# Performance work log

Hardware: AMD Instinct MI355X
Metric: run time of the kernel (lower is better)

The kernel has to match this reference:

```python
import jax, jax.numpy as jnp
import numpy as np

A = 64        # atom_fea_len
NBR = 41      # nbr_fea_len
ORIG = 92     # orig_atom_fea_len
NCONV = 3
N = 50000     # total atoms
M = 12        # neighbors per atom
B = 1000      # crystals
NPC = 50      # atoms per crystal (B*NPC == N)
EPS = 1e-5


def setup_inputs() -> dict:
    key = jax.random.key(0)
    ks = jax.random.split(key, 16)
    s = lambda k, shape: (jax.random.normal(k, shape, jnp.float32) * 0.05)
    inp = {
        "atom_fea": jax.random.normal(ks[0], (N, ORIG), jnp.float32),
        "nbr_fea": jax.random.uniform(ks[1], (N, M, NBR), dtype=jnp.float32),
        "nbr_fea_idx": jax.random.randint(ks[2], (N, M), 0, N),
        "crystal_atom_idx": jnp.arange(B * NPC).reshape(B, NPC),
        # params (weights stored as (in, out) so fwd is x @ w + b)
        "emb_w": s(ks[3], (ORIG, A)),
        "fc_full_w": s(ks[4], (NCONV, 2 * A + NBR, 2 * A)),
        "fc_full_b": s(ks[5], (NCONV, 2 * A)),
        "bn1_g": jnp.ones((NCONV, 2 * A), jnp.float32),
        "bn1_b": jnp.zeros((NCONV, 2 * A), jnp.float32),
        "bn2_g": jnp.ones((NCONV, A), jnp.float32),
        "bn2_b": jnp.zeros((NCONV, A), jnp.float32),
        "adj_w": s(ks[6], (6, A, A)),   # torch Bilinear weight (out, in1, in2)
        "adj_b": s(ks[7], (6,)),
        "fc1_w": s(ks[8], (6, 6)),
        "fc1_b": s(ks[9], (6,)),
        "af_w": s(ks[10], (A, ORIG)),
        "af_b": s(ks[11], (ORIG,)),
    }
    return inp


def _batchnorm(x, g, b):
    # training-mode BN over axis 0 (torch default biased variance)
    m = jnp.mean(x, axis=0)
    v = jnp.var(x, axis=0)
    return (x - m) * jax.lax.rsqrt(v + EPS) * g + b


def _conv_layer(x, nbr_fea, nbr_idx, w, b, g1, b1, g2, b2):
    n, m = nbr_idx.shape
    atom_nbr = x[nbr_idx]  # (N, M, A) gather
    total = jnp.concatenate(
        [jnp.broadcast_to(x[:, None, :], (n, m, A)), atom_nbr, nbr_fea], axis=2
    )  # (N, M, 2A+NBR)
    gated = total @ w + b  # (N, M, 2A)
    gated = _batchnorm(gated.reshape(-1, 2 * A), g1, b1).reshape(n, m, 2 * A)
    nbr_filter, nbr_core = gated[..., :A], gated[..., A:]
    summed = jnp.sum(jax.nn.sigmoid(nbr_filter) * jax.nn.softplus(nbr_core), axis=1)
    summed = _batchnorm(summed, g2, b2)
    return jax.nn.softplus(x + summed)


def reference(atom_fea, nbr_fea, nbr_fea_idx, crystal_atom_idx, emb_w,
              fc_full_w, fc_full_b, bn1_g, bn1_b, bn2_g, bn2_b,
              adj_w, adj_b, fc1_w, fc1_b, af_w, af_b):
    x = atom_fea @ emb_w  # embedding, no bias
    for i in range(NCONV):
        x = _conv_layer(x, nbr_fea, nbr_fea_idx,
                        fc_full_w[i], fc_full_b[i],
                        bn1_g[i], bn1_b[i], bn2_g[i], bn2_b[i])
    cf = x[crystal_atom_idx]  # (B, NPC, A)
    # Original code bug: fc_adj(x1, x2) is called with x1 == x2 == tiled atom
    # features, so pair (i, j) depends only on atom j. Compute per-atom bilinear
    # then tile -> identical output.
    q = jnp.einsum('bnd,ode,bne->bno', cf, adj_w, cf) + adj_b  # (B, NPC, 6)
    q = q @ fc1_w + fc1_b
    logp = jax.nn.log_softmax(q, axis=-1)  # row-wise over the 6 classes
    edge_prob = jnp.broadcast_to(logp[:, None, :, :], (B, NPC, NPC, 6)).reshape(B, NPC * NPC, 6)
    atom_feature = cf @ af_w + af_b  # (B, NPC, ORIG)
    return edge_prob, atom_feature
```

## Files before the change

kernel.cpp:

```cpp
#include <hip/hip_runtime.h>
#include <hip/hip_bf16.h>

#define AA 64
#define NBRF 41
#define ORIGD 92
#define NATOM 50000
#define MM 12
#define NB 1000
#define NPCC 50
#define NEDGE (NATOM*MM)
#define NREP 64
constexpr float EPS_BN = 1e-5f;

using bf16 = __hip_bfloat16;
typedef short s16x8 __attribute__((ext_vector_type(8)));
typedef float f32x4 __attribute__((ext_vector_type(4)));

__device__ __forceinline__ float u2f(unsigned short u) {
    union { float f; unsigned int i; } v; v.i = ((unsigned int)u) << 16; return v.f;
}
__device__ __forceinline__ unsigned short f2bu(float f) {
    bf16 h = __float2bfloat16(f);
    return *reinterpret_cast<unsigned short*>(&h);
}
__device__ __forceinline__ float fsigmoid(float x) {
    float e = __expf(-x);
    return __builtin_amdgcn_rcpf(1.f + e);
}
__device__ __forceinline__ float fsoftplus(float x) {
    return fmaxf(x, 0.f) + __logf(1.f + __expf(-fabsf(x)));
}

#define GLD16(g, l)                                                              \
    __builtin_amdgcn_global_load_lds(                                            \
        (const __attribute__((address_space(1))) unsigned int*)(g),              \
        (__attribute__((address_space(3))) unsigned int*)(l), 16, 0, 0)

__global__ void k_prep0(const float* __restrict__ W, unsigned short* __restrict__ Wt,
                        float* __restrict__ stats, int nstat) {
    int b = blockIdx.x, t = threadIdx.x;
    if (b < 3) {
        for (int i = t; i < 9216; i += 256) {
            int n = i / 72, k = i - n * 72;
            float v = 0.f;
            if (b == 0)      { if (k < NBRF) v = W[(128 + k) * 128 + n]; }
            else if (b == 1) { if (k < 64)   v = W[(64 + k) * 128 + n]; }
            else             { if (k < 64)   v = W[k * 128 + n]; }
            Wt[b * 9216 + i] = f2bu(v);
        }
    } else {
        int base = (b - 3) * 2048;
        for (int i = t; i < 2048; i += 256) {
            int idx = base + i;
            if (idx < nstat) stats[idx] = 0.f;
        }
    }
}

__global__ void k_prepQ(const float* __restrict__ adjw, unsigned short* __restrict__ Bq) {
    int i = blockIdx.x * 256 + threadIdx.x;
    if (i >= 384 * 72) return;
    int n = i / 72, k = i - n * 72;
    float v = (k < 64) ? adjw[(n >> 6) * 4096 + k * 64 + (n & 63)] : 0.f;
    Bq[i] = f2bu(v);
}

__global__ __launch_bounds__(256) void k_embed(const float* __restrict__ af,
                                               const float* __restrict__ w,
                                               float* __restrict__ x,
                                               unsigned short* __restrict__ xb) {
    __shared__ float wl[ORIGD * AA];
    __shared__ float al[4][ORIGD];
    int t = threadIdx.x;
    for (int i = t; i < ORIGD * AA; i += 256) wl[i] = w[i];
    int n0 = blockIdx.x * 4;
    for (int i = t; i < 4 * ORIGD; i += 256) {
        int a = i / ORIGD, k = i - a * ORIGD;
        al[a][k] = af[(size_t)(n0 + a) * ORIGD + k];
    }
    __syncthreads();
    int c = t & 63, a = t >> 6;
    float acc = 0.f;
    #pragma unroll 4
    for (int k = 0; k < ORIGD; ++k)
        acc += al[a][k] * wl[k * AA + c];
    size_t idx = (size_t)(n0 + a) * AA + c;
    x[idx] = acc;
    xb[idx] = f2bu(acc);
}


#define MFMA_PH1(acc)                                                               \
    _Pragma("unroll")                                                               \
    for (int mt = 0; mt < 3; ++mt) {                                                \
        int mrow = w * 48 + mt * 16 + ln;                                           \
        s16x8 a0 = *reinterpret_cast<const s16x8*>(&Al[mrow * 72 + quad * 8]);      \
        s16x8 a1 = *reinterpret_cast<const s16x8*>(&Al[mrow * 72 + quad * 8 + 32]); \
        _Pragma("unroll")                                                           \
        for (int nt = 0; nt < 8; ++nt) {                                            \
            int nrow = nt * 16 + ln;                                                \
            s16x8 b0 = *reinterpret_cast<const s16x8*>(&Bl[nrow * 72 + quad * 8]);  \
            s16x8 b1 = *reinterpret_cast<const s16x8*>(&Bl[nrow * 72 + quad * 8 + 32]); \
            acc[mt][nt] = __builtin_amdgcn_mfma_f32_16x16x32_bf16(a0, b0, acc[mt][nt], 0, 0, 0); \
            acc[mt][nt] = __builtin_amdgcn_mfma_f32_16x16x32_bf16(a1, b1, acc[mt][nt], 0, 0, 0); \
        }                                                                           \
    }

__global__ __launch_bounds__(256, 2) void k_passA(const unsigned short* __restrict__ xb,
                                                  const float* __restrict__ nf,
                                                  const unsigned short* __restrict__ Wt,
                                                  const int* __restrict__ nidx,
                                                  float* __restrict__ stats,
                                                  uint4* __restrict__ gated) {
    __shared__ __attribute__((aligned(16))) unsigned char SMEM[72704];
    unsigned short* Al = reinterpret_cast<unsigned short*>(SMEM);
    unsigned short* Ax = Al + 192 * 72;
    unsigned short* As = Ax + 192 * 64;
    unsigned short* Bl = As + 16 * 64;
    int t = threadIdx.x;
    int n0 = blockIdx.x * 16;
    int w = t >> 6, lane = t & 63, ln = lane & 15, quad = lane >> 4;

    {
        const float* fg = nf + (size_t)n0 * MM * NBRF;
        #pragma unroll 4
        for (int i = t; i < 192 * NBRF; i += 256) {
            int m = i / NBRF, k = i - m * NBRF;
            Al[m * 72 + k] = f2bu(fg[i]);
        }
        #pragma unroll
        for (int i = t; i < 192 * 23; i += 256) {
            int m = i / 23, k = 41 + (i - m * 23);
            Al[m * 72 + k] = 0;
        }
    }
    for (int c = w; c < 18; c += 4)
        GLD16(Wt + c * 512 + lane * 8, (char*)Bl + c * 1024);
    const int* nb = nidx + n0 * MM;
    int idxv[6];
    #pragma unroll
    for (int c = 0; c < 6; ++c) idxv[c] = nb[w * 48 + c * 8 + (lane >> 3)];
    int sl = ((lane & 7) ^ ((lane >> 3) & 7)) * 8;
    __syncthreads();

    #pragma unroll
    for (int c = 0; c < 6; ++c)
        GLD16(xb + (size_t)idxv[c] * 64 + sl, (char*)Ax + (w * 48 + c * 8) * 128);
    if (w == 3) {
        GLD16(xb + (size_t)(n0 + (lane >> 3)) * 64 + sl, (char*)As);
        GLD16(xb + (size_t)(n0 + 8 + (lane >> 3)) * 64 + sl, (char*)As + 1024);
    }

    f32x4 acc[3][8];
    f32x4 z4 = {0.f, 0.f, 0.f, 0.f};
    for (int i = 0; i < 3; ++i) for (int j = 0; j < 8; ++j) acc[i][j] = z4;

    MFMA_PH1(acc);
    __syncthreads();
    for (int c = w; c < 18; c += 4)
        GLD16(Wt + 9216 + c * 512 + lane * 8, (char*)Bl + c * 1024);
    __syncthreads();

    {
        int sw0 = (quad ^ (ln & 7)) * 8, sw1 = ((quad + 4) ^ (ln & 7)) * 8;
        #pragma unroll
        for (int mt = 0; mt < 3; ++mt) {
            int mrow = w * 48 + mt * 16 + ln;
            s16x8 a0 = *reinterpret_cast<const s16x8*>(&Ax[mrow * 64 + sw0]);
            s16x8 a1 = *reinterpret_cast<const s16x8*>(&Ax[mrow * 64 + sw1]);
            #pragma unroll
            for (int nt = 0; nt < 8; ++nt) {
                int nrow = nt * 16 + ln;
                s16x8 b0 = *reinterpret_cast<const s16x8*>(&Bl[nrow * 72 + quad * 8]);
                s16x8 b1 = *reinterpret_cast<const s16x8*>(&Bl[nrow * 72 + quad * 8 + 32]);
                acc[mt][nt] = __builtin_amdgcn_mfma_f32_16x16x32_bf16(a0, b0, acc[mt][nt], 0, 0, 0);
                acc[mt][nt] = __builtin_amdgcn_mfma_f32_16x16x32_bf16(a1, b1, acc[mt][nt], 0, 0, 0);
            }
        }
    }
    __syncthreads();
    for (int c = w; c < 18; c += 4)
        GLD16(Wt + 2 * 9216 + c * 512 + lane * 8, (char*)Bl + c * 1024);
    __syncthreads();

    #pragma unroll
    for (int mt = 0; mt < 3; ++mt) {
        int mrow = w * 48 + mt * 16 + ln;
        int atom = mrow / 12;
        int s0 = (quad ^ (atom & 7)) * 8, s1 = ((quad + 4) ^ (atom & 7)) * 8;
        s16x8 a0 = *reinterpret_cast<const s16x8*>(&As[atom * 64 + s0]);
        s16x8 a1 = *reinterpret_cast<const s16x8*>(&As[atom * 64 + s1]);
        #pragma unroll
        for (int nt = 0; nt < 8; ++nt) {
            int nrow = nt * 16 + ln;
            s16x8 b0 = *reinterpret_cast<const s16x8*>(&Bl[nrow * 72 + quad * 8]);
            s16x8 b1 = *reinterpret_cast<const s16x8*>(&Bl[nrow * 72 + quad * 8 + 32]);
            acc[mt][nt] = __builtin_amdgcn_mfma_f32_16x16x32_bf16(a0, b0, acc[mt][nt], 0, 0, 0);
            acc[mt][nt] = __builtin_amdgcn_mfma_f32_16x16x32_bf16(a1, b1, acc[mt][nt], 0, 0, 0);
        }
    }

    uint4* gblk = gated + (size_t)blockIdx.x * 3072;
    float s[8] = {0,0,0,0,0,0,0,0}, q[8] = {0,0,0,0,0,0,0,0};
    #pragma unroll
    for (int mt = 0; mt < 3; ++mt) {
        #pragma unroll
        for (int reg = 0; reg < 4; ++reg) {
            float r[8];
            #pragma unroll
            for (int nt = 0; nt < 8; ++nt) {
                r[nt] = acc[mt][nt][reg];
                s[nt] += r[nt]; q[nt] += r[nt] * r[nt];
            }
            uint4 u;
            u.x = (unsigned)f2bu(r[0]) | ((unsigned)f2bu(r[1]) << 16);
            u.y = (unsigned)f2bu(r[2]) | ((unsigned)f2bu(r[3]) << 16);
            u.z = (unsigned)f2bu(r[4]) | ((unsigned)f2bu(r[5]) << 16);
            u.w = (unsigned)f2bu(r[6]) | ((unsigned)f2bu(r[7]) << 16);
            gblk[(mt * 4 + reg) * 256 + t] = u;
        }
    }
    #pragma unroll
    for (int nt = 0; nt < 8; ++nt) {
        s[nt] += __shfl_xor(s[nt], 16); s[nt] += __shfl_xor(s[nt], 32);
        q[nt] += __shfl_xor(q[nt], 16); q[nt] += __shfl_xor(q[nt], 32);
    }
    __syncthreads();
    float* red = reinterpret_cast<float*>(SMEM);
    if (quad == 0) {
        #pragma unroll
        for (int nt = 0; nt < 8; ++nt) {
            red[((w * 8 + nt) * 16 + ln) * 2 + 0] = s[nt];
            red[((w * 8 + nt) * 16 + ln) * 2 + 1] = q[nt];
        }
    }
    __syncthreads();
    {
        int c = t >> 1, j = t & 1;
        float v = 0.f;
        #pragma unroll
        for (int w2 = 0; w2 < 4; ++w2)
            v += red[((w2 * 8 + (c >> 4)) * 16 + (c & 15)) * 2 + j];
        int rep = (blockIdx.x & (NREP - 1)) << 8;
        atomicAdd(&stats[rep + j * 128 + c], v);
    }
}

__global__ void k_sc1(const float* __restrict__ stats, const float* __restrict__ g,
                      const float* __restrict__ b, float* __restrict__ sc) {
    int c = threadIdx.x;
    float s = 0.f, q = 0.f;
    for (int r = 0; r < NREP; ++r) {
        s += stats[r * 256 + c];
        q += stats[r * 256 + 128 + c];
    }
    float cnt = (float)NEDGE;
    float mean = s / cnt;
    float var = q / cnt - mean * mean;
    float inv = rsqrtf(var + EPS_BN);
    float scale = g[c] * inv;
    sc[c] = scale;
    sc[128 + c] = b[c] - mean * scale;
}

__global__ __launch_bounds__(256) void k_passBs(const uint4* __restrict__ gated,
                                                const float* __restrict__ sc,
                                                float* __restrict__ summed,
                                                float* __restrict__ stats2) {
    __shared__ unsigned short P[192 * 66];
    __shared__ float sred[512];
    int t = threadIdx.x;
    int n0 = blockIdx.x * 16;
    int w = t >> 6, lane = t & 63, ln = lane & 15, quad = lane >> 4;
    float scF[4], shF[4], scC[4], shC[4];
    #pragma unroll
    for (int nt = 0; nt < 4; ++nt) {
        int cc = nt * 16 + ln;
        scF[nt] = sc[cc];      shF[nt] = sc[128 + cc];
        scC[nt] = sc[64 + cc]; shC[nt] = sc[192 + cc];
    }
    const uint4* gblk = gated + (size_t)blockIdx.x * 3072;
    #pragma unroll
    for (int mt = 0; mt < 3; ++mt) {
        #pragma unroll
        for (int reg = 0; reg < 4; ++reg) {
            uint4 u = gblk[(mt * 4 + reg) * 256 + t];
            int m = (w * 3 + mt) * 16 + quad * 4 + reg;
            unsigned uu[4] = {u.x, u.y, u.z, u.w};
            #pragma unroll
            for (int nt = 0; nt < 4; ++nt) {
                float rfv = u2f((unsigned short)((nt & 1) ? (uu[nt >> 1] >> 16) : (uu[nt >> 1] & 0xffff)));
                float rcv = u2f((unsigned short)((nt & 1) ? (uu[2 + (nt >> 1)] >> 16) : (uu[2 + (nt >> 1)] & 0xffff)));
                float rf = rfv * scF[nt] + shF[nt];
                float rc = rcv * scC[nt] + shC[nt];
                P[m * 66 + nt * 16 + ln] = f2bu(fsigmoid(rf) * fsoftplus(rc));
            }
        }
    }
    __syncthreads();
    int cc = t & 63, who = t >> 6;
    float sA = 0.f, qA = 0.f;
    #pragma unroll
    for (int k2 = 0; k2 < 4; ++k2) {
        int a = who + k2 * 4;
        float v = 0.f;
        #pragma unroll
        for (int j = 0; j < 12; ++j) v += u2f(P[(a * 12 + j) * 66 + cc]);
        summed[(size_t)(n0 + a) * AA + cc] = v;
        sA += v; qA += v * v;
    }
    sred[who * 64 + cc] = sA;
    sred[256 + who * 64 + cc] = qA;
    __syncthreads();
    if (t < 64) {
        float s4 = sred[t] + sred[64 + t] + sred[128 + t] + sred[192 + t];
        float q4 = sred[256 + t] + sred[320 + t] + sred[384 + t] + sred[448 + t];
        int rep = (blockIdx.x & (NREP - 1)) << 7;
        atomicAdd(&stats2[rep + t], s4);
        atomicAdd(&stats2[rep + 64 + t], q4);
    }
}

__global__ void k_sc2(const float* __restrict__ stats2, const float* __restrict__ g,
                      const float* __restrict__ b, float* __restrict__ sc2) {
    int c = threadIdx.x;
    float s = 0.f, q = 0.f;
    for (int r = 0; r < NREP; ++r) {
        s += stats2[r * 128 + c];
        q += stats2[r * 128 + 64 + c];
    }
    float cnt = (float)NATOM;
    float mean = s / cnt;
    float var = q / cnt - mean * mean;
    float inv = rsqrtf(var + EPS_BN);
    float scale = g[c] * inv;
    sc2[c] = scale;
    sc2[64 + c] = b[c] - mean * scale;
}

__global__ void k_update(float* __restrict__ x, const float* __restrict__ summed,
                         const float* __restrict__ sc2, unsigned short* __restrict__ xb) {
    int i = blockIdx.x * blockDim.x + threadIdx.x;
    if (i < NATOM * AA) {
        int c = i & 63;
        float s = summed[i] * sc2[c] + sc2[64 + c];
        float v = fsoftplus(x[i] + s);
        x[i] = v;
        xb[i] = f2bu(v);
    }
}

__global__ __launch_bounds__(256) void k_q(const float* __restrict__ x, const int* __restrict__ cidx,
                                           const unsigned short* __restrict__ Bq,
                                           const float* __restrict__ adjb,
                                           const float* __restrict__ fc1w,
                                           const float* __restrict__ fc1b,
                                           float* __restrict__ logp) {
    __shared__ __attribute__((aligned(16))) unsigned short Aq[64 * 72];
    __shared__ __attribute__((aligned(16))) unsigned short Bl[384 * 72];
    __shared__ float qv[64][6];
    int t = threadIdx.x;
    int p0 = blockIdx.x * 64;
    for (int i = t; i < 64 * 72; i += 256) {
        int a = i / 72, k = i - a * 72;
        int ga = p0 + a;
        float v = (k < 64 && ga < NATOM) ? x[(size_t)cidx[ga < NATOM ? ga : 0] * AA + k] : 0.f;
        Aq[i] = f2bu(v);
    }
    for (int i = t; i < 3456; i += 256)
        reinterpret_cast<uint4*>(Bl)[i] = reinterpret_cast<const uint4*>(Bq)[i];
    __syncthreads();

    int w = t >> 6, lane = t & 63, ln = lane & 15, quad = lane >> 4;
    f32x4 acc[24];
    f32x4 z4 = {0.f, 0.f, 0.f, 0.f};
    #pragma unroll
    for (int i = 0; i < 24; ++i) acc[i] = z4;
    {
        int mrow = w * 16 + ln;
        s16x8 a0 = *reinterpret_cast<const s16x8*>(&Aq[mrow * 72 + quad * 8]);
        s16x8 a1 = *reinterpret_cast<const s16x8*>(&Aq[mrow * 72 + quad * 8 + 32]);
        #pragma unroll
        for (int nt = 0; nt < 24; ++nt) {
            int nrow = nt * 16 + ln;
            s16x8 b0 = *reinterpret_cast<const s16x8*>(&Bl[nrow * 72 + quad * 8]);
            s16x8 b1 = *reinterpret_cast<const s16x8*>(&Bl[nrow * 72 + quad * 8 + 32]);
            acc[nt] = __builtin_amdgcn_mfma_f32_16x16x32_bf16(a0, b0, acc[nt], 0, 0, 0);
            acc[nt] = __builtin_amdgcn_mfma_f32_16x16x32_bf16(a1, b1, acc[nt], 0, 0, 0);
        }
    }
    float cfv[4][4];
    #pragma unroll
    for (int reg = 0; reg < 4; ++reg) {
        int ga = p0 + w * 16 + quad * 4 + reg;
        const float* xr = x + (size_t)cidx[ga < NATOM ? ga : 0] * AA;
        #pragma unroll
        for (int et = 0; et < 4; ++et)
            cfv[reg][et] = (ga < NATOM) ? xr[et * 16 + ln] : 0.f;
    }
    float bo[6];
    #pragma unroll
    for (int o = 0; o < 6; ++o) bo[o] = adjb[o];
    #pragma unroll
    for (int reg = 0; reg < 4; ++reg) {
        #pragma unroll
        for (int o = 0; o < 6; ++o) {
            float p = 0.f;
            #pragma unroll
            for (int et = 0; et < 4; ++et)
                p += acc[o * 4 + et][reg] * cfv[reg][et];
            p += __shfl_xor(p, 1); p += __shfl_xor(p, 2);
            p += __shfl_xor(p, 4); p += __shfl_xor(p, 8);
            if (ln == 0) qv[w * 16 + quad * 4 + reg][o] = p + bo[o];
        }
    }
    __syncthreads();
    if (t < 64) {
        int ga = p0 + t;
        if (ga < NATOM) {
            float q2[6];
            float mx = -1e30f;
            #pragma unroll
            for (int o2 = 0; o2 < 6; ++o2) {
                float acc2 = fc1b[o2];
                #pragma unroll
                for (int o = 0; o < 6; ++o) acc2 += qv[t][o] * fc1w[o * 6 + o2];
                q2[o2] = acc2; mx = fmaxf(mx, acc2);
            }
            float se = 0.f;
            #pragma unroll
            for (int o2 = 0; o2 < 6; ++o2) se += __expf(q2[o2] - mx);
            float lse = mx + __logf(se);
            #pragma unroll
            for (int o2 = 0; o2 < 6; ++o2) logp[(size_t)ga * 6 + o2] = q2[o2] - lse;
        }
    }
}

__global__ void k_edge(const float* __restrict__ logp, float* __restrict__ out0) {
    int i4 = blockIdx.x * blockDim.x + threadIdx.x;
    if (i4 >= (NB * NPCC * NPCC * 6) / 4) return;
    int e = i4 * 4;
    int b = e / (NPCC * NPCC * 6);
    int rr = e - b * (NPCC * NPCC * 6);
    const float* lb = &logp[(size_t)b * NPCC * 6];
    float4 v;
    int r0 = rr % 300;       v.x = lb[r0];
    int r1 = (rr + 1) % 300; v.y = lb[r1];
    int r2 = (rr + 2) % 300; v.z = lb[r2];
    int r3 = (rr + 3) % 300; v.w = lb[r3];
    *reinterpret_cast<float4*>(&out0[e]) = v;
}

__global__ __launch_bounds__(256) void k_af(const float* __restrict__ x, const int* __restrict__ cidx,
                                            const float* __restrict__ afw,
                                            const float* __restrict__ afb,
                                            float* __restrict__ out1) {
    __shared__ float wl[AA * ORIGD];
    __shared__ float cfl[16][AA];
    __shared__ float bl[ORIGD];
    int t = threadIdx.x;
    for (int i = t; i < AA * ORIGD; i += 256) wl[i] = afw[i];
    if (t < ORIGD) bl[t] = afb[t];
    int p0 = blockIdx.x * 16;
    for (int i = t; i < 16 * AA; i += 256) {
        int a = i >> 6, e = i & 63;
        cfl[a][e] = x[(size_t)cidx[p0 + a] * AA + e];
    }
    __syncthreads();
    for (int i = t; i < 16 * ORIGD; i += 256) {
        int a = i / ORIGD, c = i - a * ORIGD;
        float acc = bl[c];
        #pragma unroll 8
        for (int k = 0; k < AA; ++k)
            acc += cfl[a][k] * wl[k * ORIGD + c];
        out1[(size_t)(p0 + a) * ORIGD + c] = acc;
    }
}

extern "C" void kernel_launch(void* const* d_in, const int* in_sizes, int n_in,
                              void* d_out, int out_size, void* d_ws, size_t ws_size,
                              hipStream_t stream) {
    (void)in_sizes; (void)n_in; (void)out_size; (void)ws_size;
    const float* atom_fea  = (const float*)d_in[0];
    const float* nbr_fea   = (const float*)d_in[1];
    const int*   nbr_idx   = (const int*)d_in[2];
    const int*   cidx      = (const int*)d_in[3];
    const float* emb_w     = (const float*)d_in[4];
    const float* fc_full_w = (const float*)d_in[5];
    const float* bn1_g = (const float*)d_in[7];
    const float* bn1_b = (const float*)d_in[8];
    const float* bn2_g = (const float*)d_in[9];
    const float* bn2_b = (const float*)d_in[10];
    const float* adj_w = (const float*)d_in[11];
    const float* adj_b = (const float*)d_in[12];
    const float* fc1_w = (const float*)d_in[13];
    const float* fc1_b = (const float*)d_in[14];
    const float* af_w  = (const float*)d_in[15];
    const float* af_b  = (const float*)d_in[16];

    float* out0 = (float*)d_out;
    float* out1 = out0 + (size_t)NB * NPCC * NPCC * 6;

    float* ws = (float*)d_ws;
    float* x      = ws;
    float* summed = x + (size_t)NATOM * AA;
    float* logp   = summed + (size_t)NATOM * AA;
    float* stats1 = logp + (size_t)NATOM * 6;
    float* stats2 = stats1 + (size_t)NREP * 256;
    float* sc1    = stats2 + (size_t)NREP * 128;
    float* sc2    = sc1 + 256;
    float* endf   = sc2 + 128;
    size_t off = (((size_t)((char*)endf - (char*)d_ws)) + 255) & ~(size_t)255;
    unsigned short* xb = (unsigned short*)((char*)d_ws + off);
    unsigned short* Wt = xb + (size_t)NATOM * 64;
    unsigned short* Bq = Wt + 3 * 9216;
    size_t goff = (off + ((size_t)NATOM * 64 + 3 * 9216 + 384 * 72) * 2 + 255) & ~(size_t)255;
    uint4* gated = (uint4*)((char*)d_ws + goff);

    const int nstat = NREP * 256 + NREP * 128;
    k_embed<<<NATOM / 4, 256, 0, stream>>>(atom_fea, emb_w, x, xb);
    k_prepQ<<<108, 256, 0, stream>>>(adj_w, Bq);
    for (int layer = 0; layer < 3; ++layer) {
        const float* W = fc_full_w + (size_t)layer * 169 * 128;
        k_prep0<<<15, 256, 0, stream>>>(W, Wt, stats1, nstat);
        k_passA<<<NATOM / 16, 256, 0, stream>>>(xb, nbr_fea, Wt, nbr_idx, stats1, gated);
        k_sc1<<<1, 128, 0, stream>>>(stats1, bn1_g + layer * 128, bn1_b + layer * 128, sc1);
        k_passBs<<<NATOM / 16, 256, 0, stream>>>(gated, sc1, summed, stats2);
        k_sc2<<<1, 64, 0, stream>>>(stats2, bn2_g + layer * 64, bn2_b + layer * 64, sc2);
        k_update<<<(NATOM * AA + 255) / 256, 256, 0, stream>>>(x, summed, sc2, xb);
    }
    k_q<<<(NATOM + 63) / 64, 256, 0, stream>>>(x, cidx, Bq, adj_b, fc1_w, fc1_b, logp);
    k_edge<<<((NB * NPCC * NPCC * 6) / 4 + 255) / 256, 256, 0, stream>>>(logp, out0);
    k_af<<<NATOM / 16, 256, 0, stream>>>(x, cidx, af_w, af_b, out1);
}
```

Measured before the change: 760.0 us.

## Pre-pack neighbor features to bf16 once and keep atom state only in bf16

Adds a one-time kernel that converts the fp32 neighbor features into a padded bf16 layout (48 per row), so each conv layer's passA loads them directly into LDS with async global-to-LDS copies instead of converting element by element three times. passA now prefetches both weight slices into separate LDS buffers up front and reuses one A buffer for the neighbor tile and then the gathered neighbor rows. The fp32 copy of x is dropped and every consumer reads the bf16 xb. This cuts HBM traffic but compounds bf16 rounding of the residual state across layers, which risks accuracy.

```diff
diff --git a/kernel.cpp b/kernel.cpp
--- a/kernel.cpp
+++ b/kernel.cpp
@@ -35,6 +35,26 @@
     __builtin_amdgcn_global_load_lds(                                            \
         (const __attribute__((address_space(1))) unsigned int*)(g),              \
         (__attribute__((address_space(3))) unsigned int*)(l), 16, 0, 0)
+
+__global__ __launch_bounds__(256) void k_prepN(const float* __restrict__ nf,
+                                               unsigned short* __restrict__ nbp) {
+    const int total = NEDGE * 6;
+    for (int i = blockIdx.x * 256 + threadIdx.x; i < total; i += gridDim.x * 256) {
+        int row = i / 6, j = i - row * 6;
+        const float* src = nf + (size_t)row * NBRF + j * 8;
+        int base = j * 8;
+        unsigned short h[8];
+        #pragma unroll
+        for (int e = 0; e < 8; ++e)
+            h[e] = (base + e < NBRF) ? f2bu(src[e]) : (unsigned short)0;
+        uint4 u;
+        u.x = (unsigned)h[0] | ((unsigned)h[1] << 16);
+        u.y = (unsigned)h[2] | ((unsigned)h[3] << 16);
+        u.z = (unsigned)h[4] | ((unsigned)h[5] << 16);
+        u.w = (unsigned)h[6] | ((unsigned)h[7] << 16);
+        *reinterpret_cast<uint4*>(nbp + (size_t)row * 48 + j * 8) = u;
+    }
+}
 
 __global__ void k_prep0(const float* __restrict__ W, unsigned short* __restrict__ Wt,
                         float* __restrict__ stats, int nstat) {
@@ -67,7 +87,6 @@
 
 __global__ __launch_bounds__(256) void k_embed(const float* __restrict__ af,
                                                const float* __restrict__ w,
-                                               float* __restrict__ x,
                                                unsigned short* __restrict__ xb) {
     __shared__ float wl[ORIGD * AA];
     __shared__ float al[4][ORIGD];
@@ -84,105 +103,85 @@
     #pragma unroll 4
     for (int k = 0; k < ORIGD; ++k)
         acc += al[a][k] * wl[k * AA + c];
-    size_t idx = (size_t)(n0 + a) * AA + c;
-    x[idx] = acc;
-    xb[idx] = f2bu(acc);
-}
-
-
-#define MFMA_PH1(acc)                                                               \
-    _Pragma("unroll")                                                               \
-    for (int mt = 0; mt < 3; ++mt) {                                                \
-        int mrow = w * 48 + mt * 16 + ln;                                           \
-        s16x8 a0 = *reinterpret_cast<const s16x8*>(&Al[mrow * 72 + quad * 8]);      \
-        s16x8 a1 = *reinterpret_cast<const s16x8*>(&Al[mrow * 72 + quad * 8 + 32]); \
-        _Pragma("unroll")                                                           \
-        for (int nt = 0; nt < 8; ++nt) {                                            \
-            int nrow = nt * 16 + ln;                                                \
-            s16x8 b0 = *reinterpret_cast<const s16x8*>(&Bl[nrow * 72 + quad * 8]);  \
-            s16x8 b1 = *reinterpret_cast<const s16x8*>(&Bl[nrow * 72 + quad * 8 + 32]); \
-            acc[mt][nt] = __builtin_amdgcn_mfma_f32_16x16x32_bf16(a0, b0, acc[mt][nt], 0, 0, 0); \
-            acc[mt][nt] = __builtin_amdgcn_mfma_f32_16x16x32_bf16(a1, b1, acc[mt][nt], 0, 0, 0); \
-        }                                                                           \
-    }
+    xb[(size_t)(n0 + a) * AA + c] = f2bu(acc);
+}
+
 
 __global__ __launch_bounds__(256, 2) void k_passA(const unsigned short* __restrict__ xb,
-                                                  const float* __restrict__ nf,
+                                                  const unsigned short* __restrict__ nbp,
                                                   const unsigned short* __restrict__ Wt,
                                                   const int* __restrict__ nidx,
                                                   float* __restrict__ stats,
                                                   uint4* __restrict__ gated) {
-    __shared__ __attribute__((aligned(16))) unsigned char SMEM[72704];
-    unsigned short* Al = reinterpret_cast<unsigned short*>(SMEM);
-    unsigned short* Ax = Al + 192 * 72;
-    unsigned short* As = Ax + 192 * 64;
-    unsigned short* Bl = As + 16 * 64;
+    __shared__ __attribute__((aligned(16))) unsigned char SMEM[63488];
+    unsigned short* A   = reinterpret_cast<unsigned short*>(SMEM);
+    unsigned short* As  = A + 192 * 64;
+    unsigned short* Bl0 = As + 16 * 64;
+    unsigned short* Bl1 = Bl0 + 128 * 72;
     int t = threadIdx.x;
     int n0 = blockIdx.x * 16;
     int w = t >> 6, lane = t & 63, ln = lane & 15, quad = lane >> 4;
 
-    {
-        const float* fg = nf + (size_t)n0 * MM * NBRF;
-        #pragma unroll 4
-        for (int i = t; i < 192 * NBRF; i += 256) {
-            int m = i / NBRF, k = i - m * NBRF;
-            Al[m * 72 + k] = f2bu(fg[i]);
-        }
-        #pragma unroll
-        for (int i = t; i < 192 * 23; i += 256) {
-            int m = i / 23, k = 41 + (i - m * 23);
-            Al[m * 72 + k] = 0;
-        }
-    }
+    const unsigned short* nbrow = nbp + (size_t)n0 * MM * 48;
     for (int c = w; c < 18; c += 4)
-        GLD16(Wt + c * 512 + lane * 8, (char*)Bl + c * 1024);
-    const int* nb = nidx + n0 * MM;
-    int idxv[6];
-    #pragma unroll
-    for (int c = 0; c < 6; ++c) idxv[c] = nb[w * 48 + c * 8 + (lane >> 3)];
+        GLD16(nbrow + c * 512 + lane * 8, (char*)A + c * 1024);
+    for (int c = w; c < 18; c += 4)
+        GLD16(Wt + c * 512 + lane * 8, (char*)Bl0 + c * 1024);
+    for (int c = w; c < 18; c += 4)
+        GLD16(Wt + 9216 + c * 512 + lane * 8, (char*)Bl1 + c * 1024);
     int sl = ((lane & 7) ^ ((lane >> 3) & 7)) * 8;
-    __syncthreads();
-
-    #pragma unroll
-    for (int c = 0; c < 6; ++c)
-        GLD16(xb + (size_t)idxv[c] * 64 + sl, (char*)Ax + (w * 48 + c * 8) * 128);
     if (w == 3) {
         GLD16(xb + (size_t)(n0 + (lane >> 3)) * 64 + sl, (char*)As);
         GLD16(xb + (size_t)(n0 + 8 + (lane >> 3)) * 64 + sl, (char*)As + 1024);
     }
+    if (t < 64) A[192 * 48 + t] = 0;
+    const int* nb = nidx + n0 * MM;
+    int idxv[6];
+    #pragma unroll
+    for (int c = 0; c < 6; ++c) idxv[c] = nb[w * 48 + c * 8 + (lane >> 3)];
+    __syncthreads();
 
     f32x4 acc[3][8];
     f32x4 z4 = {0.f, 0.f, 0.f, 0.f};
     for (int i = 0; i < 3; ++i) for (int j = 0; j < 8; ++j) acc[i][j] = z4;
-
-    MFMA_PH1(acc);
-    __syncthreads();
+    int sw0 = (quad ^ (ln & 7)) * 8, sw1 = ((quad + 4) ^ (ln & 7)) * 8;
+
+    #pragma unroll
+    for (int mt = 0; mt < 3; ++mt) {
+        int mrow = w * 48 + mt * 16 + ln;
+        s16x8 a0 = *reinterpret_cast<const s16x8*>(&A[mrow * 48 + quad * 8]);
+        s16x8 a1 = *reinterpret_cast<const s16x8*>(&A[mrow * 48 + quad * 8 + 32]);
+        #pragma unroll
+        for (int nt = 0; nt < 8; ++nt) {
+            int nrow = nt * 16 + ln;
+            s16x8 b0 = *reinterpret_cast<const s16x8*>(&Bl0[nrow * 72 + quad * 8]);
+            s16x8 b1 = *reinterpret_cast<const s16x8*>(&Bl0[nrow * 72 + quad * 8 + 32]);
+            acc[mt][nt] = __builtin_amdgcn_mfma_f32_16x16x32_bf16(a0, b0, acc[mt][nt], 0, 0, 0);
+            acc[mt][nt] = __builtin_amdgcn_mfma_f32_16x16x32_bf16(a1, b1, acc[mt][nt], 0, 0, 0);
+        }
+    }
+    __syncthreads();
+    #pragma unroll
+    for (int c = 0; c < 6; ++c)
+        GLD16(xb + (size_t)idxv[c] * 64 + sl, (char*)A + (w * 48 + c * 8) * 128);
     for (int c = w; c < 18; c += 4)
-        GLD16(Wt + 9216 + c * 512 + lane * 8, (char*)Bl + c * 1024);
-    __syncthreads();
-
-    {
-        int sw0 = (quad ^ (ln & 7)) * 8, sw1 = ((quad + 4) ^ (ln & 7)) * 8;
-        #pragma unroll
-        for (int mt = 0; mt < 3; ++mt) {
-            int mrow = w * 48 + mt * 16 + ln;
-            s16x8 a0 = *reinterpret_cast<const s16x8*>(&Ax[mrow * 64 + sw0]);
-            s16x8 a1 = *reinterpret_cast<const s16x8*>(&Ax[mrow * 64 + sw1]);
-            #pragma unroll
-            for (int nt = 0; nt < 8; ++nt) {
-                int nrow = nt * 16 + ln;
-                s16x8 b0 = *reinterpret_cast<const s16x8*>(&Bl[nrow * 72 + quad * 8]);
-                s16x8 b1 = *reinterpret_cast<const s16x8*>(&Bl[nrow * 72 + quad * 8 + 32]);
-                acc[mt][nt] = __builtin_amdgcn_mfma_f32_16x16x32_bf16(a0, b0, acc[mt][nt], 0, 0, 0);
-                acc[mt][nt] = __builtin_amdgcn_mfma_f32_16x16x32_bf16(a1, b1, acc[mt][nt], 0, 0, 0);
-            }
-        }
-    }
-    __syncthreads();
-    for (int c = w; c < 18; c += 4)
-        GLD16(Wt + 2 * 9216 + c * 512 + lane * 8, (char*)Bl + c * 1024);
-    __syncthreads();
-
+        GLD16(Wt + 2 * 9216 + c * 512 + lane * 8, (char*)Bl0 + c * 1024);
+    __syncthreads();
+
+    #pragma unroll
+    for (int mt = 0; mt < 3; ++mt) {
+        int mrow = w * 48 + mt * 16 + ln;
+        s16x8 a0 = *reinterpret_cast<const s16x8*>(&A[mrow * 64 + sw0]);
+        s16x8 a1 = *reinterpret_cast<const s16x8*>(&A[mrow * 64 + sw1]);
+        #pragma unroll
+        for (int nt = 0; nt < 8; ++nt) {
+            int nrow = nt * 16 + ln;
+            s16x8 b0 = *reinterpret_cast<const s16x8*>(&Bl1[nrow * 72 + quad * 8]);
+            s16x8 b1 = *reinterpret_cast<const s16x8*>(&Bl1[nrow * 72 + quad * 8 + 32]);
+            acc[mt][nt] = __builtin_amdgcn_mfma_f32_16x16x32_bf16(a0, b0, acc[mt][nt], 0, 0, 0);
+            acc[mt][nt] = __builtin_amdgcn_mfma_f32_16x16x32_bf16(a1, b1, acc[mt][nt], 0, 0, 0);
+        }
+    }
     #pragma unroll
     for (int mt = 0; mt < 3; ++mt) {
         int mrow = w * 48 + mt * 16 + ln;
@@ -193,8 +192,8 @@
         #pragma unroll
         for (int nt = 0; nt < 8; ++nt) {
             int nrow = nt * 16 + ln;
-            s16x8 b0 = *reinterpret_cast<const s16x8*>(&Bl[nrow * 72 + quad * 8]);
-            s16x8 b1 = *reinterpret_cast<const s16x8*>(&Bl[nrow * 72 + quad * 8 + 32]);
+            s16x8 b0 = *reinterpret_cast<const s16x8*>(&Bl0[nrow * 72 + quad * 8]);
+            s16x8 b1 = *reinterpret_cast<const s16x8*>(&Bl0[nrow * 72 + quad * 8 + 32]);
             acc[mt][nt] = __builtin_amdgcn_mfma_f32_16x16x32_bf16(a0, b0, acc[mt][nt], 0, 0, 0);
             acc[mt][nt] = __builtin_amdgcn_mfma_f32_16x16x32_bf16(a1, b1, acc[mt][nt], 0, 0, 0);
         }
@@ -338,19 +337,18 @@
     sc2[64 + c] = b[c] - mean * scale;
 }
 
-__global__ void k_update(float* __restrict__ x, const float* __restrict__ summed,
-                         const float* __restrict__ sc2, unsigned short* __restrict__ xb) {
+__global__ void k_update(unsigned short* __restrict__ xb, const float* __restrict__ summed,
+                         const float* __restrict__ sc2) {
     int i = blockIdx.x * blockDim.x + threadIdx.x;
     if (i < NATOM * AA) {
         int c = i & 63;
         float s = summed[i] * sc2[c] + sc2[64 + c];
-        float v = fsoftplus(x[i] + s);
-        x[i] = v;
-        xb[i] = f2bu(v);
-    }
-}
-
-__global__ __launch_bounds__(256) void k_q(const float* __restrict__ x, const int* __restrict__ cidx,
+        xb[i] = f2bu(fsoftplus(u2f(xb[i]) + s));
+    }
+}
+
+__global__ __launch_bounds__(256) void k_q(const unsigned short* __restrict__ xb,
+                                           const int* __restrict__ cidx,
                                            const unsigned short* __restrict__ Bq,
                                            const float* __restrict__ adjb,
                                            const float* __restrict__ fc1w,
@@ -364,8 +362,8 @@
     for (int i = t; i < 64 * 72; i += 256) {
         int a = i / 72, k = i - a * 72;
         int ga = p0 + a;
-        float v = (k < 64 && ga < NATOM) ? x[(size_t)cidx[ga < NATOM ? ga : 0] * AA + k] : 0.f;
-        Aq[i] = f2bu(v);
+        Aq[i] = (k < 64 && ga < NATOM)
+            ? xb[(size_t)cidx[ga < NATOM ? ga : 0] * AA + k] : (unsigned short)0;
     }
     for (int i = t; i < 3456; i += 256)
         reinterpret_cast<uint4*>(Bl)[i] = reinterpret_cast<const uint4*>(Bq)[i];
@@ -393,10 +391,10 @@
     #pragma unroll
     for (int reg = 0; reg < 4; ++reg) {
         int ga = p0 + w * 16 + quad * 4 + reg;
-        const float* xr = x + (size_t)cidx[ga < NATOM ? ga : 0] * AA;
+        const unsigned short* xr = xb + (size_t)cidx[ga < NATOM ? ga : 0] * AA;
         #pragma unroll
         for (int et = 0; et < 4; ++et)
-            cfv[reg][et] = (ga < NATOM) ? xr[et * 16 + ln] : 0.f;
+            cfv[reg][et] = (ga < NATOM) ? u2f(xr[et * 16 + ln]) : 0.f;
     }
     float bo[6];
     #pragma unroll
@@ -452,7 +450,8 @@
     *reinterpret_cast<float4*>(&out0[e]) = v;
 }
 
-__global__ __launch_bounds__(256) void k_af(const float* __restrict__ x, const int* __restrict__ cidx,
+__global__ __launch_bounds__(256) void k_af(const unsigned short* __restrict__ xb,
+                                            const int* __restrict__ cidx,
                                             const float* __restrict__ afw,
                                             const float* __restrict__ afb,
                                             float* __restrict__ out1) {
@@ -465,7 +464,7 @@
     int p0 = blockIdx.x * 16;
     for (int i = t; i < 16 * AA; i += 256) {
         int a = i >> 6, e = i & 63;
-        cfl[a][e] = x[(size_t)cidx[p0 + a] * AA + e];
+        cfl[a][e] = u2f(xb[(size_t)cidx[p0 + a] * AA + e]);
     }
     __syncthreads();
     for (int i = t; i < 16 * ORIGD; i += 256) {
@@ -503,8 +502,7 @@
     float* out1 = out0 + (size_t)NB * NPCC * NPCC * 6;
 
     float* ws = (float*)d_ws;
-    float* x      = ws;
-    float* summed = x + (size_t)NATOM * AA;
+    float* summed = ws;
     float* logp   = summed + (size_t)NATOM * AA;
     float* stats1 = logp + (size_t)NATOM * 6;
     float* stats2 = stats1 + (size_t)NREP * 256;
@@ -512,25 +510,27 @@
     float* sc2    = sc1 + 256;
     float* endf   = sc2 + 128;
     size_t off = (((size_t)((char*)endf - (char*)d_ws)) + 255) & ~(size_t)255;
-    unsigned short* xb = (unsigned short*)((char*)d_ws + off);
-    unsigned short* Wt = xb + (size_t)NATOM * 64;
-    unsigned short* Bq = Wt + 3 * 9216;
-    size_t goff = (off + ((size_t)NATOM * 64 + 3 * 9216 + 384 * 72) * 2 + 255) & ~(size_t)255;
+    unsigned short* xb  = (unsigned short*)((char*)d_ws + off);
+    unsigned short* Wt  = xb + (size_t)NATOM * 64;
+    unsigned short* Bq  = Wt + 3 * 9216;
+    unsigned short* nbp = Bq + 384 * 72;
+    size_t goff = (off + ((size_t)NATOM * 64 + 3 * 9216 + 384 * 72 + (size_t)NEDGE * 48) * 2 + 255) & ~(size_t)255;
     uint4* gated = (uint4*)((char*)d_ws + goff);
 
     const int nstat = NREP * 256 + NREP * 128;
-    k_embed<<<NATOM / 4, 256, 0, stream>>>(atom_fea, emb_w, x, xb);
+    k_prepN<<<2048, 256, 0, stream>>>(nbr_fea, nbp);
+    k_embed<<<NATOM / 4, 256, 0, stream>>>(atom_fea, emb_w, xb);
     k_prepQ<<<108, 256, 0, stream>>>(adj_w, Bq);
     for (int layer = 0; layer < 3; ++layer) {
         const float* W = fc_full_w + (size_t)layer * 169 * 128;
         k_prep0<<<15, 256, 0, stream>>>(W, Wt, stats1, nstat);
-        k_passA<<<NATOM / 16, 256, 0, stream>>>(xb, nbr_fea, Wt, nbr_idx, stats1, gated);
+        k_passA<<<NATOM / 16, 256, 0, stream>>>(xb, nbp, Wt, nbr_idx, stats1, gated);
         k_sc1<<<1, 128, 0, stream>>>(stats1, bn1_g + layer * 128, bn1_b + layer * 128, sc1);
         k_passBs<<<NATOM / 16, 256, 0, stream>>>(gated, sc1, summed, stats2);
         k_sc2<<<1, 64, 0, stream>>>(stats2, bn2_g + layer * 64, bn2_b + layer * 64, sc2);
-        k_update<<<(NATOM * AA + 255) / 256, 256, 0, stream>>>(x, summed, sc2, xb);
-    }
-    k_q<<<(NATOM + 63) / 64, 256, 0, stream>>>(x, cidx, Bq, adj_b, fc1_w, fc1_b, logp);
+        k_update<<<(NATOM * AA + 255) / 256, 256, 0, stream>>>(xb, summed, sc2);
+    }
+    k_q<<<(NATOM + 63) / 64, 256, 0, stream>>>(xb, cidx, Bq, adj_b, fc1_w, fc1_b, logp);
     k_edge<<<((NB * NPCC * NPCC * 6) / 4 + 255) / 256, 256, 0, stream>>>(logp, out0);
-    k_af<<<NATOM / 16, 256, 0, stream>>>(x, cidx, af_w, af_b, out1);
-}
+    k_af<<<NATOM / 16, 256, 0, stream>>>(xb, cidx, af_w, af_b, out1);
+}
```

Result: faster. 708.3 us (-6.8%).
